# Kernel optimization log

Hardware: AMD Instinct MI355X
Metric: run time of the kernel (lower is better)

Reference implementation:

```python
import jax, jax.numpy as jnp
import numpy as np

GRID_SIZE = 5
SPLINE_ORDER = 3
B, D, O = 16384, 512, 512


def _make_grid():
    h = 2.0 / GRID_SIZE
    # matches torch.arange(-k, grid_size + k + 1) * h - 2.0  -> 12 knots
    return jnp.arange(-SPLINE_ORDER, GRID_SIZE + SPLINE_ORDER + 1, dtype=jnp.float32) * h - 2.0


def _bspline_basis(x, grid):
    # x: [B, D]; grid: [G] with G = grid_size + 2*order + 1 = 12
    G = grid.shape[0]
    xe = x[..., None]                      # [B, D, 1]
    g = grid.reshape(1, 1, G)              # [1, 1, G]
    # degree-0: indicator of knot interval  -> [B, D, G-1]
    bases = ((xe >= g[:, :, :-1]) & (xe < g[:, :, 1:])).astype(x.dtype)
    eps = 1e-9
    for k in range(1, SPLINE_ORDER + 1):   # Cox-de Boor recursion, width shrinks by 1 each step
        left = (xe - g[:, :, :-k - 1]) / (g[:, :, k:-1] - g[:, :, :-k - 1] + eps)
        right = (g[:, :, k + 1:] - xe) / (g[:, :, k + 1:] - g[:, :, 1:-k] + eps)
        bases = left * bases[..., :-1] + right * bases[..., 1:]
    return bases                           # [B, D, grid_size + order] = [B, D, 8]


def setup_inputs() -> dict:
    key = jax.random.key(0)
    k1, k2, k3 = jax.random.split(key, 3)
    x = jax.random.normal(k1, (B, D), dtype=jnp.float32)
    # kaiming_uniform_(a=sqrt(5)*0.1): bound = sqrt(6 / ((1 + a^2) * fan_in))
    a = np.sqrt(5.0) * 0.1
    bound = float(np.sqrt(6.0 / ((1.0 + a * a) * D)))
    base_weight = jax.random.uniform(k2, (O, D), dtype=jnp.float32, minval=-bound, maxval=bound)
    spline_weight = jax.random.normal(k3, (O, D, GRID_SIZE + SPLINE_ORDER), dtype=jnp.float32) * 0.01
    return {"x": x, "base_weight": base_weight, "spline_weight": spline_weight}


def reference(x, base_weight, spline_weight):
    grid = _make_grid()
    base_output = jnp.matmul(jax.nn.silu(x), base_weight.T)      # [B, O]
    x_norm = jnp.clip(x, -2.0, 2.0)
    basis = _bspline_basis(x_norm, grid)                          # [B, D, 8]
    spline_output = jnp.einsum('bic,oic->bo', basis, spline_weight)
    return base_output + spline_output
```

## Files before the change

### kernel.cpp

```cpp
#include <hip/hip_runtime.h>
#include <cstdint>
#include <cstddef>
#include <type_traits>

#define B_ROWS 16384
#define D_DIM  512
#define O_DIM  512
#define K_DIM  4608
#define BM 64
#define BN 256
#define BK 32

typedef __bf16 bf16;
typedef __attribute__((ext_vector_type(8))) bf16  bf16x8;
typedef __attribute__((ext_vector_type(4))) float f32x4;

__device__ __forceinline__ void async_load16(const void* g, void* l) {
    __builtin_amdgcn_global_load_lds(
        (const __attribute__((address_space(1))) void*)g,
        (__attribute__((address_space(3))) void*)l,
        16, 0, 0);
}

__device__ __forceinline__ uint32_t pk2(float a, float b) {
    uint16_t ua = __builtin_bit_cast(uint16_t, (__bf16)a);
    uint16_t ub = __builtin_bit_cast(uint16_t, (__bf16)b);
    return (uint32_t)ua | ((uint32_t)ub << 16);
}

__device__ __forceinline__ void spline_pairs(float xv, uint32_t out[4]) {
    float xn = fminf(fmaxf(xv, -2.0f), 2.0f);
    float t  = (xn + 3.2f) * 2.5f;
    int   j0 = (int)t;
    float u  = t - (float)j0;
    float u2 = u * u, u3 = u2 * u, omu = 1.0f - u;
    const float s6 = 1.0f / 6.0f;
    float w0 = omu * omu * omu * s6;
    float w1 = (3.0f * u3 - 6.0f * u2 + 4.0f) * s6;
    float w2 = (-3.0f * u3 + 3.0f * u2 + 3.0f * u + 1.0f) * s6;
    float w3 = u3 * s6;
    uint64_t W64 = ((uint64_t)pk2(w2, w3) << 32) | pk2(w0, w1);
    int sh = (j0 - 3) * 16;
    uint64_t lo = W64 << (sh & 63);
    uint64_t hi = W64 >> ((64 - sh) & 63);
    uint32_t lo_lo = (uint32_t)lo, lo_hi = (uint32_t)(lo >> 32);
    uint32_t hi_lo = (uint32_t)hi, hi_hi = (uint32_t)(hi >> 32);
    bool lt64 = sh < 64, eq0 = (sh == 0), lt128 = sh < 128;
    out[0] = lt64 ? lo_lo : 0u;
    out[1] = lt64 ? lo_hi : 0u;
    out[2] = lt64 ? (eq0 ? 0u : hi_lo) : (lt128 ? lo_lo : 0u);
    out[3] = lt64 ? (eq0 ? 0u : hi_hi) : (lt128 ? lo_hi : 0u);
}

__global__ void pack_w_kernel(const float* __restrict__ bw,
                              const float* __restrict__ sw,
                              bf16* __restrict__ W) {
    int idx = blockIdx.x * blockDim.x + threadIdx.x;
    if (idx >= O_DIM * 64) return;
    int o  = idx >> 6;
    int i0 = (idx & 63) * 8;

    bf16 ob[9][8];
    const float* bwp = bw + (size_t)o * D_DIM + i0;
#pragma unroll
    for (int e = 0; e < 8; e++) {
        ob[0][e] = (bf16)bwp[e];
        const float* sp = sw + ((size_t)o * D_DIM + i0 + e) * 8;
#pragma unroll
        for (int c = 0; c < 8; c++)
            ob[c + 1][e] = (bf16)sp[c];
    }
    bf16* row = W + (size_t)o * K_DIM + i0;
#pragma unroll
    for (int f = 0; f < 9; f++)
        *(bf16x8*)(row + (size_t)f * D_DIM) = *(const bf16x8*)ob[f];
}

__global__ __launch_bounds__(256, 2)
void gemm_fused_kernel(const float* __restrict__ x, const bf16* __restrict__ W,
                       float* __restrict__ C) {
    __shared__ __align__(16) bf16 As0[BM * BK];
    __shared__ __align__(16) bf16 As1[BM * BK];
    __shared__ __align__(16) bf16 Bs0[BN * BK];
    __shared__ __align__(16) bf16 Bs1[BN * BK];

    const int tid  = threadIdx.x;
    const int n0   = blockIdx.x * BN;
    const int m0   = blockIdx.y * BM;
    const int wave = tid >> 6;
    const int lane = tid & 63;
    const int wn   = wave * 64;
    const int l15  = lane & 15;
    const int quad = lane >> 4;

    const int rA = tid >> 2;
    const int q8 = tid & 3;
    const float* xrow = x + (size_t)(m0 + rA) * D_DIM + q8 * 8;
    const int aslot = q8 ^ ((rA >> 1) & 3);
    const int awo = rA * BK + aslot * 8;
    bf16* aw0 = &As0[awo];
    bf16* aw1 = &As1[awo];

    const int sr = tid >> 2;
    const int sc = ((tid & 3) ^ ((sr >> 1) & 3)) * 8;
    const bf16* gB = W + (size_t)(n0 + sr) * K_DIM + sc;
    bf16* lb0 = &Bs0[tid * 8];
    bf16* lb1 = &Bs1[tid * 8];

    const int swz  = (l15 >> 1) & 3;
    const int aoff = l15 * BK + (quad ^ swz) * 8;
    const int boff = (wn + l15) * BK + (quad ^ swz) * 8;

    f32x4 acc[4][4] = {};
    uint32_t vpk[2][4][8];
    float xe[8];

    {
        float4 a = *(const float4*)xrow;
        float4 b = *(const float4*)(xrow + 4);
        xe[0]=a.x; xe[1]=a.y; xe[2]=a.z; xe[3]=a.w;
        xe[4]=b.x; xe[5]=b.y; xe[6]=b.z; xe[7]=b.w;
#pragma unroll
        for (int e = 0; e < 8; e++) {
            uint32_t o4[4];
            spline_pairs(xe[e], o4);
            vpk[0][0][e]=o4[0]; vpk[0][1][e]=o4[1];
            vpk[0][2][e]=o4[2]; vpk[0][3][e]=o4[3];
        }
        float sl[8];
#pragma unroll
        for (int e = 0; e < 8; e++)
            sl[e] = xe[e] * __builtin_amdgcn_rcpf(1.0f + __expf(-xe[e]));
        uint32_t o[4] = {pk2(sl[0],sl[1]), pk2(sl[2],sl[3]),
                         pk2(sl[4],sl[5]), pk2(sl[6],sl[7])};
        *(uint4*)aw0 = *(const uint4*)o;
#pragma unroll
        for (int j = 0; j < 4; j++)
            async_load16(gB + (size_t)j * 64 * K_DIM, lb0 + j * 2048);
    }
    __syncthreads();

    auto chunk_body = [&](auto pcv, int c) {
        constexpr int PC = decltype(pcv)::value;
#pragma unroll
        for (int f = 0; f < 9; f++) {
            constexpr_int:;
            const int cur = (PC + f) & 1;
            const bf16* Asr = cur ? As1 : As0;
            const bf16* Bsr = cur ? Bs1 : Bs0;
            bf16* lbn = cur ? lb0 : lb1;
            bf16* awn = cur ? aw0 : aw1;
            const bool haveNext = !(c == 15 && f == 8);

            bf16x8 af[4], bfr[4];
#pragma unroll
            for (int tt = 0; tt < 4; tt++)
                af[tt] = *(const bf16x8*)(Asr + aoff + tt * 16 * BK);
#pragma unroll
            for (int tt = 0; tt < 4; tt++)
                bfr[tt] = *(const bf16x8*)(Bsr + boff + tt * 16 * BK);

            if (haveNext) {
                int koff = (f < 8) ? ((f + 1) * D_DIM + c * 32) : ((c + 1) * 32);
#pragma unroll
                for (int j = 0; j < 4; j++)
                    async_load16(gB + (size_t)j * 64 * K_DIM + koff, lbn + j * 2048);
            }
            if (f == 0 && c < 15) {
                float4 a = *(const float4*)(xrow + (c + 1) * 32);
                float4 b = *(const float4*)(xrow + (c + 1) * 32 + 4);
                xe[0]=a.x; xe[1]=a.y; xe[2]=a.z; xe[3]=a.w;
                xe[4]=b.x; xe[5]=b.y; xe[6]=b.z; xe[7]=b.w;
            }
            if (f >= 1 && c < 15) {
                uint32_t o4[4];
                spline_pairs(xe[f - 1], o4);
                vpk[PC ^ 1][0][f-1]=o4[0]; vpk[PC ^ 1][1][f-1]=o4[1];
                vpk[PC ^ 1][2][f-1]=o4[2]; vpk[PC ^ 1][3][f-1]=o4[3];
            }
            if (haveNext) {
                uint32_t o[4];
                if (f < 8) {
                    const int pr = f >> 1;
#pragma unroll
                    for (int m = 0; m < 4; m++) {
                        uint32_t lo = vpk[PC][pr][2*m], hi = vpk[PC][pr][2*m+1];
                        o[m] = (f & 1) ? ((lo >> 16) | (hi & 0xFFFF0000u))
                                       : ((lo & 0xFFFFu) | (hi << 16));
                    }
                } else {
                    float sl[8];
#pragma unroll
                    for (int e = 0; e < 8; e++)
                        sl[e] = xe[e] * __builtin_amdgcn_rcpf(1.0f + __expf(-xe[e]));
                    o[0]=pk2(sl[0],sl[1]); o[1]=pk2(sl[2],sl[3]);
                    o[2]=pk2(sl[4],sl[5]); o[3]=pk2(sl[6],sl[7]);
                }
                *(uint4*)awn = *(const uint4*)o;
            }

#pragma unroll
            for (int im = 0; im < 4; im++)
#pragma unroll
                for (int jn = 0; jn < 4; jn++)
                    acc[im][jn] = __builtin_amdgcn_mfma_f32_16x16x32_bf16(
                        af[im], bfr[jn], acc[im][jn], 0, 0, 0);
            __syncthreads();
        }
    };

    for (int cc = 0; cc < 16; cc += 2) {
        chunk_body(std::integral_constant<int,0>{}, cc);
        chunk_body(std::integral_constant<int,1>{}, cc + 1);
    }

#pragma unroll
    for (int im = 0; im < 4; im++) {
        const int rbase = m0 + im * 16 + quad * 4;
#pragma unroll
        for (int jn = 0; jn < 4; jn++) {
            const int col = n0 + wn + jn * 16 + l15;
#pragma unroll
            for (int rr = 0; rr < 4; rr++)
                C[(size_t)(rbase + rr) * O_DIM + col] = acc[im][jn][rr];
        }
    }
}

extern "C" void kernel_launch(void* const* d_in, const int* in_sizes, int n_in,
                              void* d_out, int out_size, void* d_ws, size_t ws_size,
                              hipStream_t stream) {
    const float* x  = (const float*)d_in[0];
    const float* bw = (const float*)d_in[1];
    const float* sw = (const float*)d_in[2];
    float* out = (float*)d_out;

    const size_t Wbytes = (size_t)O_DIM * K_DIM * sizeof(bf16);
    if (ws_size < Wbytes) return;
    bf16* W = (bf16*)d_ws;

    pack_w_kernel<<<(O_DIM * 64 + 255) / 256, 256, 0, stream>>>(bw, sw, W);
    gemm_fused_kernel<<<dim3(O_DIM / BN, B_ROWS / BM), 256, 0, stream>>>(x, W, out);
}
```

Baseline: 184.0 us.

## Enlarge GEMM tile to 128x256 with 8 waves and triple-buffered B prefetch

Doubles the M tile to 128 rows using 512 threads (2x4 wave grid), so each B tile loaded into LDS is reused across twice as many rows. The B operand is now triple-buffered, with global-to-LDS loads issued two steps ahead and partial vmcnt waits fused with barriers in place of full __syncthreads. MFMA sections are wrapped with s_setprio, and the grid becomes 1D. This targets memory latency and W traffic per output, at the cost of more LDS and threads per block, which may lower occupancy.

```diff
diff --git a/kernel.cpp b/kernel.cpp
--- a/kernel.cpp
+++ b/kernel.cpp
@@ -7,7 +7,7 @@
 #define D_DIM  512
 #define O_DIM  512
 #define K_DIM  4608
-#define BM 64
+#define BM 128
 #define BN 256
 #define BK 32
 
@@ -76,40 +76,38 @@
         *(bf16x8*)(row + (size_t)f * D_DIM) = *(const bf16x8*)ob[f];
 }
 
-__global__ __launch_bounds__(256, 2)
+#define BARW(n) asm volatile("s_waitcnt vmcnt(" #n ") lgkmcnt(0)\n\ts_barrier" ::: "memory")
+
+__global__ __launch_bounds__(512, 2)
 void gemm_fused_kernel(const float* __restrict__ x, const bf16* __restrict__ W,
                        float* __restrict__ C) {
     __shared__ __align__(16) bf16 As0[BM * BK];
     __shared__ __align__(16) bf16 As1[BM * BK];
     __shared__ __align__(16) bf16 Bs0[BN * BK];
     __shared__ __align__(16) bf16 Bs1[BN * BK];
+    __shared__ __align__(16) bf16 Bs2[BN * BK];
 
     const int tid  = threadIdx.x;
-    const int n0   = blockIdx.x * BN;
-    const int m0   = blockIdx.y * BM;
+    const int bid  = blockIdx.x;
+    const int n0   = (bid & 1) * BN;
+    const int m0   = (bid >> 1) * BM;
     const int wave = tid >> 6;
     const int lane = tid & 63;
-    const int wn   = wave * 64;
+    const int wm   = (wave >> 2) * 64;
+    const int wn   = (wave & 3) * 64;
     const int l15  = lane & 15;
     const int quad = lane >> 4;
+    const int swz  = (l15 >> 1) & 3;
+    const int aoff = l15 * BK + (quad ^ swz) * 8;
+    const int boff = (wn + l15) * BK + (quad ^ swz) * 8;
 
     const int rA = tid >> 2;
     const int q8 = tid & 3;
     const float* xrow = x + (size_t)(m0 + rA) * D_DIM + q8 * 8;
-    const int aslot = q8 ^ ((rA >> 1) & 3);
-    const int awo = rA * BK + aslot * 8;
-    bf16* aw0 = &As0[awo];
-    bf16* aw1 = &As1[awo];
-
-    const int sr = tid >> 2;
-    const int sc = ((tid & 3) ^ ((sr >> 1) & 3)) * 8;
-    const bf16* gB = W + (size_t)(n0 + sr) * K_DIM + sc;
-    bf16* lb0 = &Bs0[tid * 8];
-    bf16* lb1 = &Bs1[tid * 8];
-
-    const int swz  = (l15 >> 1) & 3;
-    const int aoff = l15 * BK + (quad ^ swz) * 8;
-    const int boff = (wn + l15) * BK + (quad ^ swz) * 8;
+    const int awo = rA * BK + ((q8 ^ ((rA >> 1) & 3)) * 8);
+
+    const bf16* gB = W + (size_t)(n0 + (tid >> 2)) * K_DIM
+                       + (((tid & 3) ^ ((tid >> 3) & 3)) * 8);
 
     f32x4 acc[4][4] = {};
     uint32_t vpk[2][4][8];
@@ -120,6 +118,10 @@
         float4 b = *(const float4*)(xrow + 4);
         xe[0]=a.x; xe[1]=a.y; xe[2]=a.z; xe[3]=a.w;
         xe[4]=b.x; xe[5]=b.y; xe[6]=b.z; xe[7]=b.w;
+        async_load16(gB,                             &Bs0[tid * 8]);
+        async_load16(gB + (size_t)128 * K_DIM,       &Bs0[tid * 8 + 4096]);
+        async_load16(gB + 512,                       &Bs1[tid * 8]);
+        async_load16(gB + 512 + (size_t)128 * K_DIM, &Bs1[tid * 8 + 4096]);
 #pragma unroll
         for (int e = 0; e < 8; e++) {
             uint32_t o4[4];
@@ -133,45 +135,46 @@
             sl[e] = xe[e] * __builtin_amdgcn_rcpf(1.0f + __expf(-xe[e]));
         uint32_t o[4] = {pk2(sl[0],sl[1]), pk2(sl[2],sl[3]),
                          pk2(sl[4],sl[5]), pk2(sl[6],sl[7])};
-        *(uint4*)aw0 = *(const uint4*)o;
-#pragma unroll
-        for (int j = 0; j < 4; j++)
-            async_load16(gB + (size_t)j * 64 * K_DIM, lb0 + j * 2048);
-    }
-    __syncthreads();
+        *(uint4*)(As0 + awo) = *(const uint4*)o;
+        BARW(2);
+    }
 
     auto chunk_body = [&](auto pcv, int c) {
         constexpr int PC = decltype(pcv)::value;
 #pragma unroll
         for (int f = 0; f < 9; f++) {
-            constexpr_int:;
-            const int cur = (PC + f) & 1;
-            const bf16* Asr = cur ? As1 : As0;
-            const bf16* Bsr = cur ? Bs1 : Bs0;
-            bf16* lbn = cur ? lb0 : lb1;
-            bf16* awn = cur ? aw0 : aw1;
+            const int rb = (PC + f) & 1;
+            const bf16* Asr = rb ? As1 : As0;
+            bf16*       Asw = rb ? As0 : As1;
+            const int bb = f % 3;
+            const int pb = (f + 2) % 3;
+            const bf16* Bsr = (bb == 0) ? Bs0 : (bb == 1) ? Bs1 : Bs2;
+            bf16*       Bsw = (pb == 0) ? Bs0 : (pb == 1) ? Bs1 : Bs2;
             const bool haveNext = !(c == 15 && f == 8);
 
-            bf16x8 af[4], bfr[4];
-#pragma unroll
-            for (int tt = 0; tt < 4; tt++)
-                af[tt] = *(const bf16x8*)(Asr + aoff + tt * 16 * BK);
-#pragma unroll
-            for (int tt = 0; tt < 4; tt++)
-                bfr[tt] = *(const bf16x8*)(Bsr + boff + tt * 16 * BK);
-
-            if (haveNext) {
-                int koff = (f < 8) ? ((f + 1) * D_DIM + c * 32) : ((c + 1) * 32);
-#pragma unroll
-                for (int j = 0; j < 4; j++)
-                    async_load16(gB + (size_t)j * 64 * K_DIM + koff, lbn + j * 2048);
-            }
             if (f == 0 && c < 15) {
                 float4 a = *(const float4*)(xrow + (c + 1) * 32);
                 float4 b = *(const float4*)(xrow + (c + 1) * 32 + 4);
                 xe[0]=a.x; xe[1]=a.y; xe[2]=a.z; xe[3]=a.w;
                 xe[4]=b.x; xe[5]=b.y; xe[6]=b.z; xe[7]=b.w;
             }
+            {
+                const int f2 = (f + 2) % 9;
+                const int c2 = c + (f >= 7);
+                if (c2 < 16) {
+                    const bf16* src = gB + (size_t)(f2 * 512 + c2 * 32);
+                    async_load16(src,                       &Bsw[tid * 8]);
+                    async_load16(src + (size_t)128 * K_DIM, &Bsw[tid * 8 + 4096]);
+                }
+            }
+            bf16x8 af[4], bfr[4];
+#pragma unroll
+            for (int tt = 0; tt < 4; tt++)
+                af[tt] = *(const bf16x8*)(Asr + (wm + tt * 16) * BK + aoff);
+#pragma unroll
+            for (int tt = 0; tt < 4; tt++)
+                bfr[tt] = *(const bf16x8*)(Bsr + boff + tt * 16 * BK);
+
             if (f >= 1 && c < 15) {
                 uint32_t o4[4];
                 spline_pairs(xe[f - 1], o4);
@@ -196,16 +199,27 @@
                     o[0]=pk2(sl[0],sl[1]); o[1]=pk2(sl[2],sl[3]);
                     o[2]=pk2(sl[4],sl[5]); o[3]=pk2(sl[6],sl[7]);
                 }
-                *(uint4*)awn = *(const uint4*)o;
-            }
-
+                *(uint4*)(Asw + awo) = *(const uint4*)o;
+            }
+
+            __builtin_amdgcn_s_setprio(1);
 #pragma unroll
             for (int im = 0; im < 4; im++)
 #pragma unroll
                 for (int jn = 0; jn < 4; jn++)
                     acc[im][jn] = __builtin_amdgcn_mfma_f32_16x16x32_bf16(
                         af[im], bfr[jn], acc[im][jn], 0, 0, 0);
-            __syncthreads();
+            __builtin_amdgcn_s_setprio(0);
+
+            if (f == 0) {
+                if (c < 15) { BARW(4); } else { BARW(2); }
+            } else if (f == 7) {
+                if (c < 15) { BARW(2); } else { BARW(0); }
+            } else if (f == 8) {
+                if (c < 15) { BARW(2); }
+            } else {
+                BARW(2);
+            }
         }
     };
 
@@ -216,7 +230,7 @@
 
 #pragma unroll
     for (int im = 0; im < 4; im++) {
-        const int rbase = m0 + im * 16 + quad * 4;
+        const int rbase = m0 + wm + im * 16 + quad * 4;
 #pragma unroll
         for (int jn = 0; jn < 4; jn++) {
             const int col = n0 + wn + jn * 16 + l15;
@@ -240,5 +254,5 @@
     bf16* W = (bf16*)d_ws;
 
     pack_w_kernel<<<(O_DIM * 64 + 255) / 256, 256, 0, stream>>>(bw, sw, W);
-    gemm_fused_kernel<<<dim3(O_DIM / BN, B_ROWS / BM), 256, 0, stream>>>(x, W, out);
-}
+    gemm_fused_kernel<<<dim3(B_ROWS / BM * (O_DIM / BN)), dim3(512), 0, stream>>>(x, W, out);
+}
```

New measurement: 180.2 us. 1.02x faster.
